# Optimization experiments

Measured on AMD Instinct MI355X. Metric: run time of the kernel, lower is better.

The kernel has to match this reference:

```python
import jax, jax.numpy as jnp
import numpy as np

HEADS = 16


def setup_inputs() -> dict:
    key = jax.random.key(0)
    ks = jax.random.split(key, 6)
    B, S, D = 2, 2048, 1024
    return {
        "x": jax.random.normal(ks[0], (B, S, D), dtype=jnp.float32),
        "q_in": jax.random.normal(ks[1], (B, S, D), dtype=jnp.float32),
        "WQ": jax.random.normal(ks[2], (D, D), dtype=jnp.float32) * 0.03,
        "WK": jax.random.normal(ks[3], (D, D), dtype=jnp.float32) * 0.03,
        "WV": jax.random.normal(ks[4], (D, D), dtype=jnp.float32) * 0.03,
        "WO": jax.random.normal(ks[5], (D, D), dtype=jnp.float32) * 0.03,
    }


def reference(x, q_in, WQ, WK, WV, WO):
    B, S, D = x.shape
    H = HEADS
    hd = D // H
    # projections; tf.split on last dim == reshape to (B,S,H,hd)
    Q = (q_in @ WQ).reshape(B, S, H, hd)
    K = (x @ WK).reshape(B, S, H, hd)
    V = (x @ WV).reshape(B, S, H, hd)
    scores = jnp.einsum("bqhd,bkhd->bhqk", Q, K)  # [B,H,S,S]
    # causal additive mask: 0 on/below diagonal, -inf above
    causal = jnp.tril(jnp.ones((S, S), dtype=bool))
    mask = jnp.where(causal, 0.0, -jnp.inf).astype(scores.dtype)
    # NOTE: original adds the mask BEFORE scaling, and scales by sqrt(d_model)
    attn = jax.nn.softmax((scores + mask) / np.sqrt(D).astype(scores.dtype), axis=-1)
    ctx = jnp.einsum("bhqk,bkhd->bqhd", attn, V).reshape(B, S, D)
    return ctx @ WO
```

## Files before the change

kernel.cpp:

```cpp
#include <hip/hip_runtime.h>


typedef __bf16 bf16_t;
typedef __attribute__((ext_vector_type(8))) __bf16 bf16x8;
typedef __attribute__((ext_vector_type(4))) __bf16 bf16x4;
typedef __attribute__((ext_vector_type(4))) float f32x4;

#define SCALE_LOG2E 0.045084220027780106f
#define FIXED_MAX 8.0f

__device__ __forceinline__ void async_load16(const void* g, void* l) {
  __builtin_amdgcn_global_load_lds(
      (const __attribute__((address_space(1))) void*)g,
      (__attribute__((address_space(3))) void*)l, 16, 0, 0);
}

__global__ void prep(const float* __restrict__ x, const float* __restrict__ q,
                     const float* __restrict__ w0, const float* __restrict__ w1,
                     const float* __restrict__ w2, const float* __restrict__ w3,
                     bf16_t* __restrict__ xb, bf16_t* __restrict__ qb,
                     bf16_t* __restrict__ wt) {
  const int bid = blockIdx.x;
  if (bid < 4096) {
    const float* src = (bid >= 2048) ? q : x;
    bf16_t* dst = (bid >= 2048) ? qb : xb;
    const size_t i = ((size_t)(bid & 2047) * 256 + threadIdx.x) * 8;
    float4 v0 = *(const float4*)(src + i);
    float4 v1 = *(const float4*)(src + i + 4);
    bf16x8 o;
    o[0] = (bf16_t)v0.x; o[1] = (bf16_t)v0.y; o[2] = (bf16_t)v0.z; o[3] = (bf16_t)v0.w;
    o[4] = (bf16_t)v1.x; o[5] = (bf16_t)v1.y; o[6] = (bf16_t)v1.z; o[7] = (bf16_t)v1.w;
    *(bf16x8*)(dst + i) = o;
  } else {
    const int wb = bid - 4096;
    const int z = wb >> 8;
    const float* W = z == 0 ? w0 : z == 1 ? w1 : z == 2 ? w2 : w3;
    bf16_t* dst = wt + (size_t)z * 1048576;
    const int r0 = ((wb >> 4) & 15) * 64, c0 = (wb & 15) * 64;
    __shared__ bf16_t t[64][72];
#pragma unroll
    for (int i = 0; i < 16; ++i) {
      int flat = i * 256 + threadIdx.x;
      int r = flat >> 6, c = flat & 63;
      t[c][r] = (bf16_t)W[(size_t)(r0 + r) * 1024 + c0 + c];
    }
    __syncthreads();
    const int c = threadIdx.x >> 2, seg = (threadIdx.x & 3) * 16;
    bf16x8 a = *(const bf16x8*)&t[c][seg];
    bf16x8 b = *(const bf16x8*)&t[c][seg + 8];
    bf16_t* drow = dst + (size_t)(c0 + c) * 1024 + r0 + seg;
    *(bf16x8*)drow = a;
    *(bf16x8*)(drow + 8) = b;
  }
}

template <int MODE>
__global__ __launch_bounds__(256, MODE == 2 ? 4 : 3) void gemm128(
    const bf16_t* __restrict__ Aq, const bf16_t* __restrict__ Ax,
    const bf16_t* __restrict__ Bt,
    bf16_t* __restrict__ Cq, bf16_t* __restrict__ Cvt, float* __restrict__ Cf) {
  constexpr int K = 1024;
  constexpr int NT = (MODE == 2) ? 2 : 4;
  constexpr int NROWS = NT * 32;
  const int n0 = blockIdx.x * NROWS;
  const int m0 = blockIdx.y * 128;
  const bf16_t* A = (MODE == 0 && n0 >= 1024) ? Ax : Aq;

  __shared__ bf16_t lA[128 * 64];
  __shared__ bf16_t lB[NROWS * 64];

  const int tid = threadIdx.x;
  const int w = tid >> 6, l = tid & 63;
  const int wm = (w & 1) * 64, wn = (w >> 1) * (NT * 16);
  const int fr = l & 15, fq = l >> 4;
  const int xr = fr & 7;
  const int srow = l >> 3;
  const int swz = ((l & 7) ^ srow) * 8;

  const int gk0 = (fq ^ xr) * 8;
  const int gk1 = ((4 + fq) ^ xr) * 8;

  f32x4 acc[4][NT] = {};

  for (int kt = 0; kt < K; kt += 64) {
    __syncthreads();
#pragma unroll
    for (int c = 0; c < 4; ++c) {
      const int ch = w * 4 + c;
      async_load16(A + (size_t)(m0 + ch * 8 + srow) * K + kt + swz, &lA[ch * 512]);
      if (NT == 4) {
        async_load16(Bt + (size_t)(n0 + ch * 8 + srow) * K + kt + swz, &lB[ch * 512]);
      } else if (c < 2) {
        const int bch = w * 2 + c;
        async_load16(Bt + (size_t)(n0 + bch * 8 + srow) * K + kt + swz, &lB[bch * 512]);
      }
    }
    __syncthreads();
    bf16x8 af[4][2], bfr[NT][2];
#pragma unroll
    for (int i = 0; i < 4; ++i) {
      const int row = (wm + i * 16 + fr) * 64;
      af[i][0] = *(const bf16x8*)&lA[row + gk0];
      af[i][1] = *(const bf16x8*)&lA[row + gk1];
    }
#pragma unroll
    for (int j = 0; j < NT; ++j) {
      const int row = (wn + j * 16 + fr) * 64;
      bfr[j][0] = *(const bf16x8*)&lB[row + gk0];
      bfr[j][1] = *(const bf16x8*)&lB[row + gk1];
    }
#pragma unroll
    for (int i = 0; i < 4; ++i)
#pragma unroll
      for (int j = 0; j < NT; ++j) {
        acc[i][j] = __builtin_amdgcn_mfma_f32_16x16x32_bf16(af[i][0], bfr[j][0], acc[i][j], 0, 0, 0);
        acc[i][j] = __builtin_amdgcn_mfma_f32_16x16x32_bf16(af[i][1], bfr[j][1], acc[i][j], 0, 0, 0);
      }
  }

  if (MODE == 2) {
#pragma unroll
    for (int i = 0; i < 4; ++i) {
      const int m = m0 + wm + i * 16 + fq * 4;
#pragma unroll
      for (int j = 0; j < NT; ++j) {
        const int n = n0 + wn + j * 16 + fr;
#pragma unroll
        for (int r = 0; r < 4; ++r) Cf[(size_t)(m + r) * 1024 + n] = acc[i][j][r];
      }
    }
  } else if (n0 < 2048) {
#pragma unroll
    for (int i = 0; i < 4; ++i) {
      const int m = m0 + wm + i * 16 + fq * 4;
#pragma unroll
      for (int j = 0; j < NT; ++j) {
        const int n = n0 + wn + j * 16 + fr;
#pragma unroll
        for (int r = 0; r < 4; ++r) Cq[(size_t)(m + r) * 3072 + n] = (bf16_t)acc[i][j][r];
      }
    }
  } else {
#pragma unroll
    for (int i = 0; i < 4; ++i) {
      const int mb = m0 + wm + i * 16 + fq * 4;
      const int bb = mb >> 11, ss = mb & 2047;
#pragma unroll
      for (int j = 0; j < NT; ++j) {
        const int nn = n0 - 2048 + wn + j * 16 + fr;
        const int hh = nn >> 6, dd = nn & 63;
        bf16x4 pk;
#pragma unroll
        for (int r = 0; r < 4; ++r) pk[r] = (bf16_t)acc[i][j][r];
        *(bf16x4*)(Cvt + (size_t)((bb * 16 + hh) * 64 + dd) * 2048 + ss) = pk;
      }
    }
  }
}

__global__ __launch_bounds__(512, 4) void attn8w(const bf16_t* __restrict__ qkv,
                                                 const bf16_t* __restrict__ vt,
                                                 bf16_t* __restrict__ ctx) {
  const int p = blockIdx.y;
  const int bh = blockIdx.x;
  const int b = bh >> 4, h = bh & 15;
  const int tid = threadIdx.x, w = tid >> 6, l = tid & 63;
  const int fr = l & 15, fq = l >> 4;
  const int qq4 = w & 3;
  const int kh = w >> 2;

  __shared__ __align__(16) bf16_t lK[2][64 * 64];
  __shared__ __align__(16) bf16_t lV[2][64 * 64];
  __shared__ __align__(16) bf16_t lP[8][16 * 40];
  __shared__ __align__(16) float lRed[4][16][68];

  const bf16_t* kg = qkv + (size_t)b * 2048 * 3072 + 1024 + h * 64;
  const bf16_t* vg = vt + (size_t)(b * 16 + h) * 64 * 2048;

  const int srow = l >> 3;
  const int swz = ((l & 7) ^ srow) * 8;
  const int xr = fr & 7;

  const int kbase = (kh * 32 + fr) * 64;
  const int g0 = (fq ^ xr) * 8, g1 = ((4 + fq) ^ xr) * 8;
  const int vbase = fr * 64;
  const int vg0 = ((kh * 4 + fq) ^ xr) * 8;
  const int pwr = fr * 40 + fq * 4;
  const int prd = fr * 40 + fq * 8;
  bf16_t* lPw = &lP[w][0];

  bf16x8 ones;
#pragma unroll
  for (int i = 0; i < 8; ++i) ones[i] = (bf16_t)1.0f;

#pragma unroll 1
  for (int phase = 0; phase < 2; ++phase) {
    const int qt = (phase == 0) ? (16 + p) : (15 - p);
    const int qw = qt * 64 + qq4 * 16;

    bf16x8 qf[2];
#pragma unroll
    for (int ks = 0; ks < 2; ++ks)
      qf[ks] = *(const bf16x8*)(qkv + (size_t)(b * 2048 + qw + fr) * 3072 +
                                h * 64 + ks * 32 + fq * 8);

    f32x4 o[4] = {};
    f32x4 liacc = {};

    const bf16_t* kp = kg + (size_t)(w * 8 + srow) * 3072 + swz;
    const bf16_t* vp = vg + (size_t)(w * 8 + srow) * 2048 + swz;

    if (phase == 1) __syncthreads();
    async_load16(kp, &lK[0][w * 512]);
    async_load16(vp, &lV[0][w * 512]);
    kp += 64 * 3072;
    vp += 64;

    auto compute = [&](int kt, int buf) {
      const int kb = kt * 64 + kh * 32;
      if (kb > qw + 15) return;
      const bf16_t* lKb = &lK[buf][0];
      const bf16_t* lVb = &lV[buf][0];
      f32x4 s[2] = {};
#pragma unroll
      for (int t = 0; t < 2; ++t) {
        bf16x8 k0 = *(const bf16x8*)&lKb[kbase + t * 1024 + g0];
        bf16x8 k1 = *(const bf16x8*)&lKb[kbase + t * 1024 + g1];
        s[t] = __builtin_amdgcn_mfma_f32_16x16x32_bf16(k0, qf[0], s[t], 0, 0, 0);
        s[t] = __builtin_amdgcn_mfma_f32_16x16x32_bf16(k1, qf[1], s[t], 0, 0, 0);
      }
      const int qq = qw + fr;
      const bool needmask = (kb + 31) > qw;
#pragma unroll
      for (int t = 0; t < 2; ++t) {
        bf16x4 pk;
#pragma unroll
        for (int r = 0; r < 4; ++r) {
          float v = fmaf(s[t][r], SCALE_LOG2E, -FIXED_MAX);
          if (needmask && (kb + t * 16 + fq * 4 + r > qq)) v = -1e30f;
          pk[r] = (bf16_t)__builtin_amdgcn_exp2f(v);
        }
        *(bf16x4*)&lPw[pwr + t * 16] = pk;
      }
      bf16x8 pf = *(const bf16x8*)&lPw[prd];
#pragma unroll
      for (int dt = 0; dt < 4; ++dt) {
        bf16x8 vf = *(const bf16x8*)&lVb[vbase + dt * 1024 + vg0];
        o[dt] = __builtin_amdgcn_mfma_f32_16x16x32_bf16(vf, pf, o[dt], 0, 0, 0);
      }
      liacc = __builtin_amdgcn_mfma_f32_16x16x32_bf16(ones, pf, liacc, 0, 0, 0);
    };

    int kt = 0;
#pragma unroll 1
    while (true) {
      __syncthreads();
      if (kt < qt) {
        async_load16(kp, &lK[1][w * 512]);
        async_load16(vp, &lV[1][w * 512]);
        kp += 64 * 3072; vp += 64;
      }
      compute(kt, 0);
      if (++kt > qt) break;
      __syncthreads();
      if (kt < qt) {
        async_load16(kp, &lK[0][w * 512]);
        async_load16(vp, &lV[0][w * 512]);
        kp += 64 * 3072; vp += 64;
      }
      compute(kt, 1);
      if (++kt > qt) break;
    }

    __syncthreads();
    if (kh) {
#pragma unroll
      for (int dt = 0; dt < 4; ++dt)
        *(f32x4*)&lRed[qq4][fr][dt * 16 + fq * 4] = o[dt];
      if (fq == 0) lRed[qq4][fr][64] = liacc[0];
    }
    __syncthreads();
    if (!kh) {
      const float lsum = liacc[0] + lRed[qq4][fr][64];
      const float inv = 1.f / lsum;
      bf16_t* cb = ctx + (size_t)(b * 2048 + qw + fr) * 1024 + h * 64;
#pragma unroll
      for (int dt = 0; dt < 4; ++dt) {
        f32x4 v = o[dt] + *(f32x4*)&lRed[qq4][fr][dt * 16 + fq * 4];
        bf16x4 ov;
#pragma unroll
        for (int r = 0; r < 4; ++r) ov[r] = (bf16_t)(v[r] * inv);
        *(bf16x4*)(cb + dt * 16 + fq * 4) = ov;
      }
    }
  }
}

extern "C" void kernel_launch(void* const* d_in, const int* in_sizes, int n_in,
                              void* d_out, int out_size, void* d_ws, size_t ws_size,
                              hipStream_t stream) {
  const float* x  = (const float*)d_in[0];
  const float* q  = (const float*)d_in[1];
  const float* WQ = (const float*)d_in[2];
  const float* WK = (const float*)d_in[3];
  const float* WV = (const float*)d_in[4];
  const float* WO = (const float*)d_in[5];
  float* out = (float*)d_out;

  bf16_t* qb  = (bf16_t*)d_ws;
  bf16_t* xb  = qb + 4194304;
  bf16_t* wt  = xb + 4194304;
  bf16_t* qkv = wt + 4194304;
  bf16_t* vtp = qkv + (size_t)4096 * 3072;
  bf16_t* ctx = vtp + 4194304;

  prep<<<dim3(5120), 256, 0, stream>>>(x, q, WQ, WK, WV, WO, xb, qb, wt);
  gemm128<0><<<dim3(24, 32), 256, 0, stream>>>(qb, xb, wt, qkv, vtp, nullptr);
  attn8w<<<dim3(32, 16), 512, 0, stream>>>(qkv, vtp, ctx);
  gemm128<2><<<dim3(16, 32), 256, 0, stream>>>(ctx, ctx, wt + (size_t)3072 * 1024,
                                               nullptr, nullptr, out);
}
```

Before: 181.0 us.

## Replace QKV projection GEMM with double-buffered 256x256 tile kernel

Adds a new QKV projection kernel that uses 256x256 output tiles, 512 threads and double-buffered LDS. Async global-to-LDS loads for later K tiles are issued in phases interleaved with the MFMA work, using explicit waitcnt, barriers and setprio to overlap memory with compute. Larger tiles raise data reuse per block. The trade-offs are heavier LDS use (128KB), fewer blocks (192) for the 256 CUs, and fragile hand-written synchronisation. The old gemm128 is reduced to the output-projection path only.

Result: slower. 186.8 us (+3.2%).

```diff
diff --git a/kernel.cpp b/kernel.cpp
--- a/kernel.cpp
+++ b/kernel.cpp
@@ -54,17 +54,140 @@
   }
 }
 
+__global__ __launch_bounds__(512) void gemm256(
+    const bf16_t* __restrict__ Aq, const bf16_t* __restrict__ Ax,
+    const bf16_t* __restrict__ Bt,
+    bf16_t* __restrict__ Cq, bf16_t* __restrict__ Cvt) {
+  const int n0 = blockIdx.x * 256, m0 = blockIdx.y * 256;
+  const bf16_t* A = (blockIdx.x < 4) ? Aq : Ax;
+
+  __shared__ bf16_t lA[2][256 * 64];
+  __shared__ bf16_t lB[2][256 * 64];
+
+  const int tid = threadIdx.x, w = tid >> 6, l = tid & 63;
+  const int wrow = w & 1, wcol = w >> 1;
+  const int fr = l & 15, fq = l >> 4, xr = fr & 7;
+  const int srow = l >> 3;
+  const int swz = ((l & 7) ^ srow) * 8;
+  const int gk0 = (fq ^ xr) * 8, gk1 = ((4 + fq) ^ xr) * 8;
+
+  const int chA = (w < 4) ? w : (16 + (w - 4));
+  const int chB = w;
+
+  f32x4 acc[8][4] = {};
+
+  auto stageA = [&](int t, int u, int buf) {
+    const int ch = chA + 4 * u;
+    async_load16(A + (size_t)(m0 + ch * 8 + srow) * 1024 + t * 64 + swz,
+                 &lA[buf][ch * 512]);
+  };
+  auto stageB = [&](int t, int u, int buf) {
+    const int ch = chB + 8 * u;
+    async_load16(Bt + (size_t)(n0 + ch * 8 + srow) * 1024 + t * 64 + swz,
+                 &lB[buf][ch * 512]);
+  };
+
+#pragma unroll
+  for (int u = 0; u < 4; ++u) { stageA(0, u, 0); stageB(0, u, 0); }
+#pragma unroll
+  for (int u = 0; u < 3; ++u) { stageA(1, u, 1); stageB(1, u, 1); }
+  asm volatile("s_waitcnt vmcnt(6)" ::: "memory");
+  __builtin_amdgcn_s_barrier();
+
+  bf16x8 bf[4][2];
+
+#pragma unroll 1
+  for (int tt = 0; tt < 16; tt += 2) {
+#pragma unroll
+    for (int ph = 0; ph < 8; ++ph) {
+      const int q = ph & 3;
+      const int buf = ph >> 2;
+      if (q == 0) {
+#pragma unroll
+        for (int j = 0; j < 4; ++j) {
+          const int row = (wcol * 64 + j * 16 + fr) * 64;
+          bf[j][0] = *(const bf16x8*)&lB[buf][row + gk0];
+          bf[j][1] = *(const bf16x8*)&lB[buf][row + gk1];
+        }
+      }
+      bf16x8 af[2][2];
+#pragma unroll
+      for (int ii = 0; ii < 2; ++ii) {
+        const int row = (wrow * 128 + (q * 2 + ii) * 16 + fr) * 64;
+        af[ii][0] = *(const bf16x8*)&lA[buf][row + gk0];
+        af[ii][1] = *(const bf16x8*)&lA[buf][row + gk1];
+      }
+      {
+        int st, su, sbuf;
+        if (ph == 0)      { st = tt + 1; su = 3;      sbuf = 1; }
+        else if (ph <= 4) { st = tt + 2; su = ph - 1; sbuf = 0; }
+        else              { st = tt + 3; su = ph - 5; sbuf = 1; }
+        const int sts = (st < 16) ? st : (st - 2);
+        stageA(sts, su, sbuf);
+        stageB(sts, su, sbuf);
+      }
+      __builtin_amdgcn_s_barrier();
+      asm volatile("s_waitcnt lgkmcnt(0)" ::: "memory");
+      __builtin_amdgcn_sched_barrier(0);
+      __builtin_amdgcn_s_setprio(1);
+#pragma unroll
+      for (int ii = 0; ii < 2; ++ii)
+#pragma unroll
+        for (int j = 0; j < 4; ++j) {
+          acc[q * 2 + ii][j] = __builtin_amdgcn_mfma_f32_16x16x32_bf16(
+              af[ii][0], bf[j][0], acc[q * 2 + ii][j], 0, 0, 0);
+          acc[q * 2 + ii][j] = __builtin_amdgcn_mfma_f32_16x16x32_bf16(
+              af[ii][1], bf[j][1], acc[q * 2 + ii][j], 0, 0, 0);
+        }
+      __builtin_amdgcn_s_setprio(0);
+      __builtin_amdgcn_sched_barrier(0);
+      if (q == 3) asm volatile("s_waitcnt vmcnt(6)" ::: "memory");
+      __builtin_amdgcn_s_barrier();
+    }
+  }
+  asm volatile("s_waitcnt vmcnt(0)" ::: "memory");
+
+  if (n0 < 2048) {
+#pragma unroll
+    for (int i = 0; i < 8; ++i) {
+      const int m = m0 + wrow * 128 + i * 16 + fq * 4;
+#pragma unroll
+      for (int j = 0; j < 4; ++j) {
+        const int n = n0 + wcol * 64 + j * 16 + fr;
+#pragma unroll
+        for (int r = 0; r < 4; ++r)
+          Cq[(size_t)(m + r) * 3072 + n] = (bf16_t)acc[i][j][r];
+      }
+    }
+  } else {
+#pragma unroll
+    for (int i = 0; i < 8; ++i) {
+      const int mb = m0 + wrow * 128 + i * 16 + fq * 4;
+      const int bb = mb >> 11, ss = mb & 2047;
+#pragma unroll
+      for (int j = 0; j < 4; ++j) {
+        const int nn = n0 - 2048 + wcol * 64 + j * 16 + fr;
+        const int hh = nn >> 6, dd = nn & 63;
+        bf16x4 pk;
+#pragma unroll
+        for (int r = 0; r < 4; ++r) pk[r] = (bf16_t)acc[i][j][r];
+        *(bf16x4*)(Cvt + (size_t)((bb * 16 + hh) * 64 + dd) * 2048 + ss) = pk;
+      }
+    }
+  }
+}
+
 template <int MODE>
-__global__ __launch_bounds__(256, MODE == 2 ? 4 : 3) void gemm128(
+__global__ __launch_bounds__(256, 4) void gemm128(
     const bf16_t* __restrict__ Aq, const bf16_t* __restrict__ Ax,
     const bf16_t* __restrict__ Bt,
     bf16_t* __restrict__ Cq, bf16_t* __restrict__ Cvt, float* __restrict__ Cf) {
   constexpr int K = 1024;
-  constexpr int NT = (MODE == 2) ? 2 : 4;
+  constexpr int NT = 2;
   constexpr int NROWS = NT * 32;
   const int n0 = blockIdx.x * NROWS;
   const int m0 = blockIdx.y * 128;
-  const bf16_t* A = (MODE == 0 && n0 >= 1024) ? Ax : Aq;
+  const bf16_t* A = Aq;
 
   __shared__ bf16_t lA[128 * 64];
   __shared__ bf16_t lB[NROWS * 64];
@@ -88,9 +211,7 @@
     for (int c = 0; c < 4; ++c) {
       const int ch = w * 4 + c;
       async_load16(A + (size_t)(m0 + ch * 8 + srow) * K + kt + swz, &lA[ch * 512]);
-      if (NT == 4) {
-        async_load16(Bt + (size_t)(n0 + ch * 8 + srow) * K + kt + swz, &lB[ch * 512]);
-      } else if (c < 2) {
+      if (c < 2) {
         const int bch = w * 2 + c;
         async_load16(Bt + (size_t)(n0 + bch * 8 + srow) * K + kt + swz, &lB[bch * 512]);
       }
@@ -118,42 +239,14 @@
       }
   }
 
-  if (MODE == 2) {
-#pragma unroll
-    for (int i = 0; i < 4; ++i) {
-      const int m = m0 + wm + i * 16 + fq * 4;
-#pragma unroll
-      for (int j = 0; j < NT; ++j) {
-        const int n = n0 + wn + j * 16 + fr;
-#pragma unroll
-        for (int r = 0; r < 4; ++r) Cf[(size_t)(m + r) * 1024 + n] = acc[i][j][r];
-      }
-    }
-  } else if (n0 < 2048) {
-#pragma unroll
-    for (int i = 0; i < 4; ++i) {
-      const int m = m0 + wm + i * 16 + fq * 4;
-#pragma unroll
-      for (int j = 0; j < NT; ++j) {
-        const int n = n0 + wn + j * 16 + fr;
-#pragma unroll
-        for (int r = 0; r < 4; ++r) Cq[(size_t)(m + r) * 3072 + n] = (bf16_t)acc[i][j][r];
-      }
-    }
-  } else {
-#pragma unroll
-    for (int i = 0; i < 4; ++i) {
-      const int mb = m0 + wm + i * 16 + fq * 4;
-      const int bb = mb >> 11, ss = mb & 2047;
-#pragma unroll
-      for (int j = 0; j < NT; ++j) {
-        const int nn = n0 - 2048 + wn + j * 16 + fr;
-        const int hh = nn >> 6, dd = nn & 63;
-        bf16x4 pk;
-#pragma unroll
-        for (int r = 0; r < 4; ++r) pk[r] = (bf16_t)acc[i][j][r];
-        *(bf16x4*)(Cvt + (size_t)((bb * 16 + hh) * 64 + dd) * 2048 + ss) = pk;
-      }
+#pragma unroll
+  for (int i = 0; i < 4; ++i) {
+    const int m = m0 + wm + i * 16 + fq * 4;
+#pragma unroll
+    for (int j = 0; j < NT; ++j) {
+      const int n = n0 + wn + j * 16 + fr;
+#pragma unroll
+      for (int r = 0; r < 4; ++r) Cf[(size_t)(m + r) * 1024 + n] = acc[i][j][r];
     }
   }
 }
@@ -315,7 +408,7 @@
   bf16_t* ctx = vtp + 4194304;
 
   prep<<<dim3(5120), 256, 0, stream>>>(x, q, WQ, WK, WV, WO, xb, qb, wt);
-  gemm128<0><<<dim3(24, 32), 256, 0, stream>>>(qb, xb, wt, qkv, vtp, nullptr);
+  gemm256<<<dim3(12, 16), 512, 0, stream>>>(qb, xb, wt, qkv, vtp);
   attn8w<<<dim3(32, 16), 512, 0, stream>>>(qkv, vtp, ctx);
   gemm128<2><<<dim3(16, 32), 256, 0, stream>>>(ctx, ctx, wt + (size_t)3072 * 1024,
                                                nullptr, nullptr, out);
```
